# Performance work log

Measured on AMD Instinct MI355X. Metric: run time of the kernel, lower is better.

The kernel has to match this reference:

```python
import jax, jax.numpy as jnp
import numpy as np

N_NODES = 100000
N_EDGES = 800000
N_LABEL = 262144
IN, H, OUT = 16, 256, 128
BN_EPS = 1e-5


def setup_inputs() -> dict:
    key = jax.random.key(0)
    ks = jax.random.split(key, 32)
    def lin(k, fi, fo):
        return jax.random.normal(k, (fi, fo), jnp.float32) / np.sqrt(fi)
    inp = {
        "x": jax.random.normal(ks[0], (N_NODES, IN), jnp.float32),
        "edge_index": jax.random.randint(ks[1], (2, N_EDGES), 0, N_NODES, jnp.int32),
        "edge_weight": jax.random.uniform(ks[2], (N_EDGES,), jnp.float32),
        "edge_label_index": jax.random.randint(ks[3], (2, N_LABEL), 0, N_NODES, jnp.int32),
        # encoder GCN layers: 4 convs, BN on first 3
        "W1": lin(ks[4], IN, H),  "b1": jnp.zeros((H,), jnp.float32),
        "g1": jnp.ones((H,), jnp.float32), "be1": jnp.zeros((H,), jnp.float32),
        "W2": lin(ks[5], H, H),   "b2": jnp.zeros((H,), jnp.float32),
        "g2": jnp.ones((H,), jnp.float32), "be2": jnp.zeros((H,), jnp.float32),
        "W3": lin(ks[6], H, H),   "b3": jnp.zeros((H,), jnp.float32),
        "g3": jnp.ones((H,), jnp.float32), "be3": jnp.zeros((H,), jnp.float32),
        "W4": lin(ks[7], H, OUT), "b4": jnp.zeros((OUT,), jnp.float32),
        # decoder MLP on concatenated pair embeddings
        "D1W": lin(ks[8], 2 * OUT, OUT), "D1b": jnp.zeros((OUT,), jnp.float32),
        "D2W": lin(ks[9], OUT, OUT),     "D2b": jnp.zeros((OUT,), jnp.float32),
        "D3W": lin(ks[10], OUT, 1),      "D3b": jnp.zeros((1,), jnp.float32),
    }
    return inp


def _forward(x, edge_index, edge_weight, edge_label_index,
             W1, b1, g1, be1, W2, b2, g2, be2, W3, b3, g3, be3, W4, b4,
             D1W, D1b, D2W, D2b, D3W, D3b):
    n = x.shape[0]
    src, dst = edge_index[0], edge_index[1]
    # GCN symmetric normalization with self-loops (weight 1)
    deg = jax.ops.segment_sum(edge_weight, dst, num_segments=n) + 1.0
    dinv = jax.lax.rsqrt(deg)
    edge_norm = dinv[src] * edge_weight * dinv[dst]   # [E]
    self_norm = dinv * dinv                            # [N]

    def gcn(h, W, b):
        h = h @ W                                      # [N, F]
        agg = jax.ops.segment_sum(h[src] * edge_norm[:, None], dst, num_segments=n)
        return agg + h * self_norm[:, None] + b

    def bn(h, g, be):  # training-mode BatchNorm1d over node dim
        m = h.mean(axis=0)
        v = h.var(axis=0)
        return (h - m) * jax.lax.rsqrt(v + BN_EPS) * g + be

    h = jax.nn.relu(bn(gcn(x, W1, b1), g1, be1))
    h = jax.nn.relu(bn(gcn(h, W2, b2), g2, be2))
    h = jax.nn.relu(bn(gcn(h, W3, b3), g3, be3))
    z = gcn(h, W4, b4)                                 # [N, OUT] encoded

    # decode: gather both endpoints, concat, MLP + sigmoid
    e0, e1 = edge_label_index[0], edge_label_index[1]
    q = jnp.concatenate([z[e0], z[e1]], axis=1)        # [EL, 2*OUT]
    q = jax.nn.relu(q @ D1W + D1b)
    q = jax.nn.relu(q @ D2W + D2b)
    p = jax.nn.sigmoid(q @ D3W + D3b)
    return p.squeeze(-1)                               # [EL]


def reference(x, edge_index, edge_weight, edge_label_index,
              W1, b1, g1, be1, W2, b2, g2, be2, W3, b3, g3, be3, W4, b4,
              D1W, D1b, D2W, D2b, D3W, D3b):
    return _forward(x, edge_index, edge_weight, edge_label_index,
                    W1, b1, g1, be1, W2, b2, g2, be2, W3, b3, g3, be3, W4, b4,
                    D1W, D1b, D2W, D2b, D3W, D3b)
```

## Files before the change

### kernel.cpp

```cpp
#include <hip/hip_runtime.h>
#include <cmath>

#define NN 100000
#define NE 800000
#define NL 262144
#define GB 782

typedef __attribute__((ext_vector_type(8))) short bf16x8;
typedef __attribute__((ext_vector_type(4))) float f32x4;

__device__ __forceinline__ unsigned short f2bf(float f) {
  unsigned int u = __builtin_bit_cast(unsigned int, f);
  u = (u + 0x7FFF + ((u >> 16) & 1)) >> 16;
  return (unsigned short)u;
}
__device__ __forceinline__ float bf2f(unsigned short u) {
  return __builtin_bit_cast(float, (unsigned int)u << 16);
}

__global__ void k_degcnt(const int* __restrict__ dst, const float* __restrict__ w,
                         unsigned long long* __restrict__ dc) {
  int e = blockIdx.x * 256 + threadIdx.x;
  if (e < NE) {
    unsigned long long pk = (1ULL << 32) | (unsigned long long)(unsigned int)(w[e] * 8388608.0f);
    atomicAdd(&dc[dst[e]], pk);
  }
}
__global__ void k_dinv2(const unsigned long long* __restrict__ dc,
                        float* __restrict__ dinv, int* __restrict__ cnt) {
  int n = blockIdx.x * 256 + threadIdx.x;
  if (n < NN) {
    unsigned long long v = dc[n];
    cnt[n] = (int)(v >> 32);
    dinv[n] = rsqrtf((float)(unsigned int)v * (1.0f / 8388608.0f) + 1.0f);
  }
}
__global__ void k_scan1(const int* __restrict__ cnt, int* __restrict__ tsum) {
  __shared__ int s[256];
  int t = threadIdx.x;
  int base = blockIdx.x * 1024;
  int acc = 0;
  for (int i = 0; i < 4; i++) { int idx = base + t * 4 + i; if (idx < NN) acc += cnt[idx]; }
  s[t] = acc; __syncthreads();
  for (int o = 128; o > 0; o >>= 1) { if (t < o) s[t] += s[t + o]; __syncthreads(); }
  if (t == 0) tsum[blockIdx.x] = s[0];
}
__global__ void k_scan2(const int* __restrict__ tsum, int* __restrict__ toff, int nt, int* __restrict__ rowptr_end) {
  __shared__ int s[256];
  int t = threadIdx.x;
  int v = (t < nt) ? tsum[t] : 0;
  s[t] = v; __syncthreads();
  for (int o = 1; o < 256; o <<= 1) { int xv = (t >= o) ? s[t - o] : 0; __syncthreads(); s[t] += xv; __syncthreads(); }
  if (t < nt) toff[t] = s[t] - v;
  if (t == 255) *rowptr_end = s[255];
}
__global__ void k_scan3(const int* __restrict__ cnt, const int* __restrict__ toff,
                        int* __restrict__ rowptr, int* __restrict__ nxt) {
  __shared__ int s[256];
  int t = threadIdx.x;
  int base = blockIdx.x * 1024 + t * 4;
  int v[4]; int tot = 0;
  for (int i = 0; i < 4; i++) { int idx = base + i; v[i] = (idx < NN) ? cnt[idx] : 0; tot += v[i]; }
  s[t] = tot; __syncthreads();
  for (int o = 1; o < 256; o <<= 1) { int xv = (t >= o) ? s[t - o] : 0; __syncthreads(); s[t] += xv; __syncthreads(); }
  int excl = s[t] - tot + toff[blockIdx.x];
  for (int i = 0; i < 4; i++) {
    int idx = base + i;
    if (idx < NN) { rowptr[idx] = excl; nxt[idx] = excl; }
    excl += v[i];
  }
}
__global__ void k_scatter2(const int* __restrict__ src, const int* __restrict__ dst, const float* __restrict__ w,
                           const float* __restrict__ dinv, int* __restrict__ nxt,
                           int* __restrict__ esp, float* __restrict__ enp) {
  int e = blockIdx.x * 256 + threadIdx.x;
  if (e < NE) {
    int d = dst[e], s = src[e];
    int p = atomicAdd(&nxt[d], 1);
    esp[p] = s; enp[p] = dinv[s] * w[e] * dinv[d];
  }
}

__global__ void k_cvt_wT(const float* __restrict__ W, unsigned short* __restrict__ Wt, int K, int N) {
  int id = blockIdx.x * 256 + threadIdx.x;
  if (id >= K * N) return;
  int n = id / K, k = id - n * K;
  Wt[id] = f2bf(W[k * N + n]);
}

__global__ void k_pack(const unsigned short* __restrict__ Wt, unsigned short* __restrict__ P, int K, int NJ) {
  int id = blockIdx.x * 256 + threadIdx.x;
  int total = (K / 32) * NJ * 64;
  if (id >= total) return;
  int lane = id & 63, g = id >> 6;
  int j = g % NJ, s = g / NJ;
  int fr = lane & 15, fq = lane >> 4;
  uint4 v = *(const uint4*)(Wt + (size_t)(j * 16 + fr) * K + s * 32 + fq * 8);
  *(uint4*)(P + (size_t)id * 8) = v;
}

__global__ __launch_bounds__(256) void k_wuv(const float* __restrict__ W4, const float* __restrict__ D1W,
                                             const float* __restrict__ b4, const float* __restrict__ D1b,
                                             unsigned short* __restrict__ wtUV, float* __restrict__ buv) {
  __shared__ float dc[256];
  int j = blockIdx.x;
  int k = threadIdx.x;
  dc[k] = D1W[k * 128 + j];
  __syncthreads();
  float su = 0.f, sv = 0.f;
  const float* w4r = W4 + k * 128;
  for (int p = 0; p < 128; p++) { float w = w4r[p]; su += w * dc[p]; sv += w * dc[128 + p]; }
  wtUV[(size_t)j * 256 + k] = f2bf(su);
  wtUV[(size_t)(128 + j) * 256 + k] = f2bf(sv);
  if (k == 0) {
    float bu = D1b[j], bv = 0.f;
    for (int p = 0; p < 128; p++) { bu += b4[p] * dc[p]; bv += b4[p] * dc[128 + p]; }
    buv[j] = bu; buv[128 + j] = bv;
  }
}

__global__ __launch_bounds__(256) void k_gemm16(const float* __restrict__ x, const float* __restrict__ W,
                                                unsigned short* __restrict__ out) {
  __shared__ float xs[32][16];
  int t = threadIdx.x; int row0 = blockIdx.x * 32;
  for (int i = t; i < 512; i += 256) {
    int r = i >> 4, c = i & 15; int row = row0 + r;
    xs[r][c] = (row < NN) ? x[(size_t)row * 16 + c] : 0.f;
  }
  float w[16];
  #pragma unroll
  for (int k = 0; k < 16; k++) w[k] = W[k * 256 + t];
  __syncthreads();
  for (int r = 0; r < 32; r++) {
    int row = row0 + r; if (row >= NN) break;
    float acc = 0.f;
    #pragma unroll
    for (int k = 0; k < 16; k++) acc += xs[r][k] * w[k];
    out[(size_t)row * 256 + t] = f2bf(acc);
  }
}

template <bool STATS>
__global__ __launch_bounds__(512) void k_gemm_v8(
    const unsigned short* __restrict__ A, const unsigned short* __restrict__ Wp,
    const float* __restrict__ bias, unsigned short* __restrict__ C,
    float* __restrict__ Ps, float* __restrict__ Pq) {
  __shared__ unsigned short S[128 * 136];
  __shared__ float Ls[256], Lq[256];
  const int t = threadIdx.x;
  const int row0 = blockIdx.x * 128;
  if (STATS && t < 256) { Ls[t] = 0.f; Lq[t] = 0.f; }
  const int lane = t & 63, w = t >> 6, fr = lane & 15, fq = lane >> 4;
  f32x4 acc[16] = {};
  #pragma unroll
  for (int ck = 0; ck < 2; ck++) {
    {
      int r = t >> 2, q = t & 3;
      int row = row0 + r;
      uint4* dst = (uint4*)(S + r * 136 + q * 32);
      if (row < NN) {
        const uint4* src = (const uint4*)(A + (size_t)row * 256 + ck * 128 + q * 32);
        #pragma unroll
        for (int i = 0; i < 4; i++) dst[i] = src[i];
      } else {
        #pragma unroll
        for (int i = 0; i < 4; i++) dst[i] = make_uint4(0, 0, 0, 0);
      }
    }
    __syncthreads();
    #pragma unroll
    for (int s = 0; s < 4; s++) {
      bf16x8 a = *(const bf16x8*)(S + (w * 16 + fr) * 136 + s * 32 + fq * 8);
      const int sg = ck * 4 + s;
      #pragma unroll
      for (int j = 0; j < 16; j++) {
        bf16x8 bw = *(const bf16x8*)(Wp + ((size_t)(sg * 16 + j) * 64 + lane) * 8);
        acc[j] = __builtin_amdgcn_mfma_f32_16x16x32_bf16(a, bw, acc[j], 0, 0, 0);
      }
    }
    __syncthreads();
  }
  #pragma unroll
  for (int j = 0; j < 16; j++) {
    float bj = bias[j * 16 + fr];
    float s_ = 0.f, q_ = 0.f;
    #pragma unroll
    for (int rr = 0; rr < 4; rr++) {
      int row = row0 + w * 16 + fq * 4 + rr;
      if (row < NN) {
        float c = acc[j][rr] + bj;
        C[(size_t)row * 256 + j * 16 + fr] = f2bf(c);
        if (STATS) { s_ += c; q_ += c * c; }
      }
    }
    if (STATS) {
      s_ += __shfl_xor(s_, 16); q_ += __shfl_xor(q_, 16);
      s_ += __shfl_xor(s_, 32); q_ += __shfl_xor(q_, 32);
      if (fq == 0) { atomicAdd(&Ls[j * 16 + fr], s_); atomicAdd(&Lq[j * 16 + fr], q_); }
    }
  }
  if (STATS) {
    __syncthreads();
    if (t < 256) Ps[(size_t)blockIdx.x * 256 + t] = Ls[t];
    else Pq[(size_t)blockIdx.x * 256 + (t - 256)] = Lq[t - 256];
  }
}

__global__ __launch_bounds__(256) void k_bnred(const float* __restrict__ Ps, const float* __restrict__ Pq,
                                               const float* __restrict__ g, const float* __restrict__ be,
                                               float* __restrict__ scale, float* __restrict__ shift) {
  __shared__ float Ss[256], Sq[256];
  const int f = blockIdx.x;
  const int t = threadIdx.x;
  float s = 0.f, q = 0.f;
  for (int p = t; p < GB; p += 256) { s += Ps[(size_t)p * 256 + f]; q += Pq[(size_t)p * 256 + f]; }
  Ss[t] = s; Sq[t] = q;
  __syncthreads();
  for (int o = 128; o > 0; o >>= 1) { if (t < o) { Ss[t] += Ss[t + o]; Sq[t] += Sq[t + o]; } __syncthreads(); }
  if (t == 0) {
    float m = Ss[0] * (1.f / NN);
    float v = Sq[0] * (1.f / NN) - m * m;
    float sc = g[f] * rsqrtf(v + 1e-5f);
    scale[f] = sc; shift[f] = be[f] - m * sc;
  }
}

__device__ __forceinline__ void ld8(const unsigned short* p, float* f) {
  uint4 v = *(const uint4*)p;
  unsigned int u[4] = {v.x, v.y, v.z, v.w};
  #pragma unroll
  for (int i = 0; i < 4; i++) {
    f[2 * i] = bf2f((unsigned short)(u[i] & 0xFFFF));
    f[2 * i + 1] = bf2f((unsigned short)(u[i] >> 16));
  }
}
template <bool BN>
__global__ __launch_bounds__(256) void k_agg5(const unsigned short* __restrict__ hb,
    const int* __restrict__ esp, const float* __restrict__ enp,
    const int* __restrict__ rowptr, const float* __restrict__ dinv,
    const float* __restrict__ scale, const float* __restrict__ shift,
    const float* __restrict__ bias, unsigned short* __restrict__ outb) {
  const int lane = threadIdx.x & 63;
  const int lg = lane & 31;
  const int srcbase = lane & 32;
  const int n = blockIdx.x * 8 + (threadIdx.x >> 5);
  const int f0 = lg * 8;
  float sc8[8] = {}, sh8[8] = {};
  if constexpr (BN) {
    #pragma unroll
    for (int j = 0; j < 8; j++) { sc8[j] = scale[f0 + j]; sh8[j] = shift[f0 + j]; }
  }
  auto xf = [&](float v, int j) -> float {
    if constexpr (BN) return fmaxf(v * sc8[j] + sh8[j], 0.f);
    else return v;
  };
  float d = dinv[n]; float dd = d * d;
  float acc[8];
  {
    float sv[8];
    ld8(hb + (size_t)n * 256 + f0, sv);
    #pragma unroll
    for (int j = 0; j < 8; j++) acc[j] = xf(sv[j], j) * dd + (BN ? 0.f : bias[f0 + j]);
  }
  const int i0 = rowptr[n];
  const int dg = rowptr[n + 1] - i0;
  int sreg = 0; float wreg = 0.f;
  if (lg < dg) { sreg = esp[i0 + lg]; wreg = enp[i0 + lg]; }
  const int m = (dg < 32) ? dg : 32;
  int e = 0;
  for (; e + 4 <= m; e += 4) {
    int s0 = __shfl(sreg, srcbase | e), s1 = __shfl(sreg, srcbase | (e + 1));
    int s2 = __shfl(sreg, srcbase | (e + 2)), s3 = __shfl(sreg, srcbase | (e + 3));
    float w0 = __shfl(wreg, srcbase | e), w1 = __shfl(wreg, srcbase | (e + 1));
    float w2 = __shfl(wreg, srcbase | (e + 2)), w3 = __shfl(wreg, srcbase | (e + 3));
    float r0[8], r1[8], r2[8], r3[8];
    ld8(hb + (size_t)s0 * 256 + f0, r0);
    ld8(hb + (size_t)s1 * 256 + f0, r1);
    ld8(hb + (size_t)s2 * 256 + f0, r2);
    ld8(hb + (size_t)s3 * 256 + f0, r3);
    #pragma unroll
    for (int j = 0; j < 8; j++)
      acc[j] += w0 * xf(r0[j], j) + w1 * xf(r1[j], j) + w2 * xf(r2[j], j) + w3 * xf(r3[j], j);
  }
  for (; e < m; e++) {
    int s0 = __shfl(sreg, srcbase | e); float w0 = __shfl(wreg, srcbase | e);
    float r0[8];
    ld8(hb + (size_t)s0 * 256 + f0, r0);
    #pragma unroll
    for (int j = 0; j < 8; j++) acc[j] += w0 * xf(r0[j], j);
  }
  for (int i = i0 + 32; i < i0 + dg; i++) {
    int s0 = esp[i]; float w0 = enp[i];
    float r0[8];
    ld8(hb + (size_t)s0 * 256 + f0, r0);
    #pragma unroll
    for (int j = 0; j < 8; j++) acc[j] += w0 * xf(r0[j], j);
  }
  unsigned int o[4];
  #pragma unroll
  for (int i = 0; i < 4; i++)
    o[i] = (unsigned int)f2bf(acc[2 * i]) | ((unsigned int)f2bf(acc[2 * i + 1]) << 16);
  *(uint4*)(outb + (size_t)n * 256 + f0) = make_uint4(o[0], o[1], o[2], o[3]);
}

__global__ __launch_bounds__(256) void k_bnstats2(const unsigned short* __restrict__ h,
                                                  float* __restrict__ sums, float* __restrict__ sqs) {
  __shared__ float L[4][256];
  int t = threadIdx.x;
  int fp = t & 127;
  size_t rbase = (size_t)blockIdx.x * 256 + (t >> 7);
  float s0 = 0, q0 = 0, s1 = 0, q1 = 0;
  for (int i = 0; i < 128; i++) {
    size_t r = rbase + 2 * (size_t)i;
    if (r >= NN) break;
    unsigned int v = *(const unsigned int*)&h[r * 256 + fp * 2];
    float a = bf2f((unsigned short)(v & 0xFFFF));
    float b = bf2f((unsigned short)(v >> 16));
    s0 += a; q0 += a * a; s1 += b; q1 += b * b;
  }
  L[0][t] = s0; L[1][t] = q0; L[2][t] = s1; L[3][t] = q1;
  __syncthreads();
  if (t < 128) {
    s0 = L[0][t] + L[0][t + 128]; q0 = L[1][t] + L[1][t + 128];
    s1 = L[2][t] + L[2][t + 128]; q1 = L[3][t] + L[3][t + 128];
    atomicAdd(&sums[2 * t], s0); atomicAdd(&sqs[2 * t], q0);
    atomicAdd(&sums[2 * t + 1], s1); atomicAdd(&sqs[2 * t + 1], q1);
  }
}
__global__ void k_bnfinal(const float* __restrict__ sums, const float* __restrict__ sqs,
                          const float* __restrict__ g, const float* __restrict__ be,
                          float* __restrict__ scale, float* __restrict__ shift) {
  int f = threadIdx.x;
  float m = sums[f] * (1.f / NN);
  float v = sqs[f] * (1.f / NN) - m * m;
  float sc = g[f] * rsqrtf(v + 1e-5f);
  scale[f] = sc; shift[f] = be[f] - m * sc;
}

__global__ __launch_bounds__(256) void k_decoder3(
    const unsigned short* __restrict__ uv,
    const int* __restrict__ l0, const int* __restrict__ l1,
    const unsigned short* __restrict__ W2p, const float* __restrict__ D2b,
    const float* __restrict__ D3W, const float* __restrict__ D3b,
    float* __restrict__ out) {
  __shared__ unsigned short S[128 * 136];
  __shared__ int ei0[128], ei1[128];
  const int t = threadIdx.x;
  const int base = blockIdx.x * 128;
  if (t < 128) ei0[t] = l0[base + t];
  else ei1[t - 128] = l1[base + t - 128];
  __syncthreads();
  {
    int e = t >> 1, h = t & 1;
    const uint4* pu = (const uint4*)(uv + (size_t)ei0[e] * 256 + h * 64);
    const uint4* pv = (const uint4*)(uv + (size_t)ei1[e] * 256 + 128 + h * 64);
    uint4* dst = (uint4*)(S + e * 136 + h * 64);
    #pragma unroll
    for (int i = 0; i < 8; i++) {
      uint4 a = pu[i], b = pv[i];
      unsigned int ia[4] = {a.x, a.y, a.z, a.w};
      unsigned int ib[4] = {b.x, b.y, b.z, b.w};
      unsigned int o[4];
      #pragma unroll
      for (int p = 0; p < 4; p++) {
        float lo = fmaxf(bf2f((unsigned short)(ia[p] & 0xFFFF)) + bf2f((unsigned short)(ib[p] & 0xFFFF)), 0.f);
        float hi = fmaxf(bf2f((unsigned short)(ia[p] >> 16)) + bf2f((unsigned short)(ib[p] >> 16)), 0.f);
        o[p] = (unsigned int)f2bf(lo) | ((unsigned int)f2bf(hi) << 16);
      }
      dst[i] = make_uint4(o[0], o[1], o[2], o[3]);
    }
  }
  __syncthreads();
  const int lane = t & 63, w = t >> 6, fr = lane & 15, fq = lane >> 4;
  f32x4 acc2[2][8] = {};
  #pragma unroll
  for (int s = 0; s < 4; s++) {
    bf16x8 a0 = *(const bf16x8*)(S + (w * 32 + fr) * 136 + s * 32 + fq * 8);
    bf16x8 a1 = *(const bf16x8*)(S + (w * 32 + 16 + fr) * 136 + s * 32 + fq * 8);
    #pragma unroll
    for (int j = 0; j < 8; j++) {
      bf16x8 bw = *(const bf16x8*)(W2p + ((size_t)(s * 8 + j) * 64 + lane) * 8);
      acc2[0][j] = __builtin_amdgcn_mfma_f32_16x16x32_bf16(a0, bw, acc2[0][j], 0, 0, 0);
      acc2[1][j] = __builtin_amdgcn_mfma_f32_16x16x32_bf16(a1, bw, acc2[1][j], 0, 0, 0);
    }
  }
  float b2v[8], w3v[8];
  #pragma unroll
  for (int j = 0; j < 8; j++) { b2v[j] = D2b[j * 16 + fr]; w3v[j] = D3W[j * 16 + fr]; }
  float d3b = D3b[0];
  #pragma unroll
  for (int f = 0; f < 2; f++) {
    float p[4] = {0.f, 0.f, 0.f, 0.f};
    #pragma unroll
    for (int j = 0; j < 8; j++)
      #pragma unroll
      for (int r = 0; r < 4; r++)
        p[r] += fmaxf(acc2[f][j][r] + b2v[j], 0.f) * w3v[j];
    #pragma unroll
    for (int r = 0; r < 4; r++) {
      p[r] += __shfl_xor(p[r], 1);
      p[r] += __shfl_xor(p[r], 2);
      p[r] += __shfl_xor(p[r], 4);
      p[r] += __shfl_xor(p[r], 8);
      if (fr == 0) out[base + w * 32 + f * 16 + fq * 4 + r] = 1.f / (1.f + expf(-(p[r] + d3b)));
    }
  }
}

extern "C" void kernel_launch(void* const* d_in, const int* in_sizes, int n_in,
                              void* d_out, int out_size, void* d_ws, size_t ws_size,
                              hipStream_t stream) {
  const float* x = (const float*)d_in[0];
  const int* ei = (const int*)d_in[1];
  const int* esrc = ei; const int* edst = ei + NE;
  const float* ew = (const float*)d_in[2];
  const int* eli = (const int*)d_in[3];
  const int* l0 = eli; const int* l1 = eli + NL;
  const float* W1 = (const float*)d_in[4],  *b1 = (const float*)d_in[5];
  const float* g1 = (const float*)d_in[6],  *be1 = (const float*)d_in[7];
  const float* W2 = (const float*)d_in[8],  *b2 = (const float*)d_in[9];
  const float* g2 = (const float*)d_in[10], *be2 = (const float*)d_in[11];
  const float* W3 = (const float*)d_in[12], *b3 = (const float*)d_in[13];
  const float* g3 = (const float*)d_in[14], *be3 = (const float*)d_in[15];
  const float* W4 = (const float*)d_in[16], *b4 = (const float*)d_in[17];
  const float* D1W = (const float*)d_in[18], *D1b = (const float*)d_in[19];
  const float* D2W = (const float*)d_in[20], *D2b = (const float*)d_in[21];
  const float* D3W = (const float*)d_in[22], *D3b = (const float*)d_in[23];
  float* out = (float*)d_out;

  float* wf = (float*)d_ws;
  size_t off = 0;
  auto A = [&](size_t n) { float* p = wf + off; off += (n + 63) & ~(size_t)63; return p; };
  float* dinv = A(NN);
  float* enp = A(NE);
  float* sums = A(256);
  float* sqs = A(256);
  float* scale = A(256);
  float* shift = A(256);
  float* buv = A(256);
  float* Ps = A((size_t)GB * 256);
  float* Pq = A((size_t)GB * 256);
  unsigned long long* dc = (unsigned long long*)A(2 * (size_t)NN);
  int* cnt = (int*)A(NN);
  int* rowptr = (int*)A(NN + 1);
  int* nxt = (int*)A(NN);
  int* esp = (int*)A(NE);
  int* tsum = (int*)A(256);
  int* toff = (int*)A(256);
  unsigned short* hbA = (unsigned short*)A((size_t)NN * 128);
  unsigned short* hbB = (unsigned short*)A((size_t)NN * 128);
  unsigned short* uv  = (unsigned short*)A((size_t)NN * 128);
  unsigned short* wt2 = (unsigned short*)A(256 * 128);
  unsigned short* wt3 = (unsigned short*)A(256 * 128);
  unsigned short* wtUV = (unsigned short*)A(256 * 128);
  unsigned short* w2t = (unsigned short*)A(64 * 128);
  unsigned short* wp2 = (unsigned short*)A(256 * 128);
  unsigned short* wp3 = (unsigned short*)A(256 * 128);
  unsigned short* wpUV = (unsigned short*)A(256 * 128);
  unsigned short* w2p = (unsigned short*)A(64 * 128);

  const int EB = (NE + 255) / 256;
  const int NB = (NN + 255) / 256;
  const int ST = (NN + 1023) / 1024;
  const int AB = NN / 8;

  hipMemsetAsync(dc, 0, (size_t)NN * 8, stream);
  k_degcnt<<<EB, 256, 0, stream>>>(edst, ew, dc);
  k_dinv2<<<NB, 256, 0, stream>>>(dc, dinv, cnt);
  k_scan1<<<ST, 256, 0, stream>>>(cnt, tsum);
  k_scan2<<<1, 256, 0, stream>>>(tsum, toff, ST, rowptr + NN);
  k_scan3<<<ST, 256, 0, stream>>>(cnt, toff, rowptr, nxt);
  k_scatter2<<<EB, 256, 0, stream>>>(esrc, edst, ew, dinv, nxt, esp, enp);

  k_cvt_wT<<<(256 * 256 + 255) / 256, 256, 0, stream>>>(W2, wt2, 256, 256);
  k_cvt_wT<<<(256 * 256 + 255) / 256, 256, 0, stream>>>(W3, wt3, 256, 256);
  k_cvt_wT<<<(128 * 128 + 255) / 256, 256, 0, stream>>>(D2W, w2t, 128, 128);
  k_wuv<<<128, 256, 0, stream>>>(W4, D1W, b4, D1b, wtUV, buv);
  k_pack<<<32, 256, 0, stream>>>(wt2, wp2, 256, 16);
  k_pack<<<32, 256, 0, stream>>>(wt3, wp3, 256, 16);
  k_pack<<<32, 256, 0, stream>>>(wtUV, wpUV, 256, 16);
  k_pack<<<8, 256, 0, stream>>>(w2t, w2p, 128, 8);

  k_gemm16<<<(NN + 31) / 32, 256, 0, stream>>>(x, W1, hbA);
  k_agg5<false><<<AB, 256, 0, stream>>>(hbA, esp, enp, rowptr, dinv, nullptr, nullptr, b1, hbB);
  hipMemsetAsync(sums, 0, 512 * sizeof(float), stream);
  k_bnstats2<<<NB, 256, 0, stream>>>(hbB, sums, sqs);
  k_bnfinal<<<1, 256, 0, stream>>>(sums, sqs, g1, be1, scale, shift);

  k_agg5<true><<<AB, 256, 0, stream>>>(hbB, esp, enp, rowptr, dinv, scale, shift, nullptr, hbA);
  k_gemm_v8<true><<<GB, 512, 0, stream>>>(hbA, wp2, b2, hbB, Ps, Pq);
  k_bnred<<<256, 256, 0, stream>>>(Ps, Pq, g2, be2, scale, shift);

  k_agg5<true><<<AB, 256, 0, stream>>>(hbB, esp, enp, rowptr, dinv, scale, shift, nullptr, hbA);
  k_gemm_v8<true><<<GB, 512, 0, stream>>>(hbA, wp3, b3, hbB, Ps, Pq);
  k_bnred<<<256, 256, 0, stream>>>(Ps, Pq, g3, be3, scale, shift);

  k_agg5<true><<<AB, 256, 0, stream>>>(hbB, esp, enp, rowptr, dinv, scale, shift, nullptr, hbA);
  k_gemm_v8<false><<<GB, 512, 0, stream>>>(hbA, wpUV, buv, uv, nullptr, nullptr);

  k_decoder3<<<NL / 128, 256, 0, stream>>>(uv, l0, l1, w2p, D2b, D3W, D3b, out);
}
```

Before: 730.4 us.

## Restructure GEMM so each wave owns column slice with register-resident weights

The GEMM kernel now loads the full 128x256 A tile into LDS at once, and each wave keeps its 32-column slice of the packed weights in registers. Previously each wave owned 16 rows and reloaded all 256 columns of weights from global memory on every k-step. The per-block BN partial sums are now written directly from the owning wave, which removes the LDS atomics and an extra barrier. The tradeoffs are higher register pressure (16 B fragments plus 16 accumulators) and more LDS per block, which may reduce occupancy.

Result: faster. 708.5 us (-3.0%).

```diff
diff --git a/kernel.cpp b/kernel.cpp
--- a/kernel.cpp
+++ b/kernel.cpp
@@ -141,68 +141,69 @@
 }
 
 template <bool STATS>
-__global__ __launch_bounds__(512) void k_gemm_v8(
+__global__ __launch_bounds__(512) void k_gemm_v12(
     const unsigned short* __restrict__ A, const unsigned short* __restrict__ Wp,
     const float* __restrict__ bias, unsigned short* __restrict__ C,
     float* __restrict__ Ps, float* __restrict__ Pq) {
-  __shared__ unsigned short S[128 * 136];
-  __shared__ float Ls[256], Lq[256];
+  __shared__ unsigned short S[128 * 264];
   const int t = threadIdx.x;
+  const int lane = t & 63, w = t >> 6, fr = lane & 15, fq = lane >> 4;
   const int row0 = blockIdx.x * 128;
-  if (STATS && t < 256) { Ls[t] = 0.f; Lq[t] = 0.f; }
-  const int lane = t & 63, w = t >> 6, fr = lane & 15, fq = lane >> 4;
-  f32x4 acc[16] = {};
-  #pragma unroll
-  for (int ck = 0; ck < 2; ck++) {
-    {
-      int r = t >> 2, q = t & 3;
-      int row = row0 + r;
-      uint4* dst = (uint4*)(S + r * 136 + q * 32);
-      if (row < NN) {
-        const uint4* src = (const uint4*)(A + (size_t)row * 256 + ck * 128 + q * 32);
-        #pragma unroll
-        for (int i = 0; i < 4; i++) dst[i] = src[i];
-      } else {
-        #pragma unroll
-        for (int i = 0; i < 4; i++) dst[i] = make_uint4(0, 0, 0, 0);
-      }
-    }
-    __syncthreads();
-    #pragma unroll
-    for (int s = 0; s < 4; s++) {
-      bf16x8 a = *(const bf16x8*)(S + (w * 16 + fr) * 136 + s * 32 + fq * 8);
-      const int sg = ck * 4 + s;
+  bf16x8 B0[8], B1[8];
+  #pragma unroll
+  for (int s = 0; s < 8; s++) {
+    B0[s] = *(const bf16x8*)(Wp + ((size_t)(s * 16 + 2 * w) * 64 + lane) * 8);
+    B1[s] = *(const bf16x8*)(Wp + ((size_t)(s * 16 + 2 * w + 1) * 64 + lane) * 8);
+  }
+  {
+    int r = t >> 2, q = t & 3;
+    int row = row0 + r;
+    uint4* dst = (uint4*)(S + r * 264 + q * 64);
+    if (row < NN) {
+      const uint4* src = (const uint4*)(A + (size_t)row * 256 + q * 64);
       #pragma unroll
-      for (int j = 0; j < 16; j++) {
-        bf16x8 bw = *(const bf16x8*)(Wp + ((size_t)(sg * 16 + j) * 64 + lane) * 8);
-        acc[j] = __builtin_amdgcn_mfma_f32_16x16x32_bf16(a, bw, acc[j], 0, 0, 0);
-      }
-    }
-    __syncthreads();
-  }
-  #pragma unroll
-  for (int j = 0; j < 16; j++) {
-    float bj = bias[j * 16 + fr];
+      for (int i = 0; i < 8; i++) dst[i] = src[i];
+    } else {
+      #pragma unroll
+      for (int i = 0; i < 8; i++) dst[i] = make_uint4(0, 0, 0, 0);
+    }
+  }
+  __syncthreads();
+  f32x4 acc[8][2] = {};
+  #pragma unroll
+  for (int r = 0; r < 8; r++) {
+    #pragma unroll
+    for (int s = 0; s < 8; s++) {
+      bf16x8 a = *(const bf16x8*)(S + (r * 16 + fr) * 264 + s * 32 + fq * 8);
+      acc[r][0] = __builtin_amdgcn_mfma_f32_16x16x32_bf16(a, B0[s], acc[r][0], 0, 0, 0);
+      acc[r][1] = __builtin_amdgcn_mfma_f32_16x16x32_bf16(a, B1[s], acc[r][1], 0, 0, 0);
+    }
+  }
+  #pragma unroll
+  for (int jl = 0; jl < 2; jl++) {
+    const int col = w * 32 + jl * 16 + fr;
+    float bj = bias[col];
     float s_ = 0.f, q_ = 0.f;
     #pragma unroll
-    for (int rr = 0; rr < 4; rr++) {
-      int row = row0 + w * 16 + fq * 4 + rr;
-      if (row < NN) {
-        float c = acc[j][rr] + bj;
-        C[(size_t)row * 256 + j * 16 + fr] = f2bf(c);
-        if (STATS) { s_ += c; q_ += c * c; }
+    for (int r = 0; r < 8; r++) {
+      #pragma unroll
+      for (int rr = 0; rr < 4; rr++) {
+        int row = row0 + r * 16 + fq * 4 + rr;
+        if (row < NN) {
+          float c = acc[r][jl][rr] + bj;
+          C[(size_t)row * 256 + col] = f2bf(c);
+          if (STATS) { s_ += c; q_ += c * c; }
+        }
       }
     }
     if (STATS) {
       s_ += __shfl_xor(s_, 16); q_ += __shfl_xor(q_, 16);
       s_ += __shfl_xor(s_, 32); q_ += __shfl_xor(q_, 32);
-      if (fq == 0) { atomicAdd(&Ls[j * 16 + fr], s_); atomicAdd(&Lq[j * 16 + fr], q_); }
-    }
-  }
-  if (STATS) {
-    __syncthreads();
-    if (t < 256) Ps[(size_t)blockIdx.x * 256 + t] = Ls[t];
-    else Pq[(size_t)blockIdx.x * 256 + (t - 256)] = Lq[t - 256];
+      if (fq == 0) {
+        Ps[(size_t)blockIdx.x * 256 + col] = s_;
+        Pq[(size_t)blockIdx.x * 256 + col] = q_;
+      }
+    }
   }
 }
 
@@ -488,15 +489,15 @@
   k_bnfinal<<<1, 256, 0, stream>>>(sums, sqs, g1, be1, scale, shift);
 
   k_agg5<true><<<AB, 256, 0, stream>>>(hbB, esp, enp, rowptr, dinv, scale, shift, nullptr, hbA);
-  k_gemm_v8<true><<<GB, 512, 0, stream>>>(hbA, wp2, b2, hbB, Ps, Pq);
+  k_gemm_v12<true><<<GB, 512, 0, stream>>>(hbA, wp2, b2, hbB, Ps, Pq);
   k_bnred<<<256, 256, 0, stream>>>(Ps, Pq, g2, be2, scale, shift);
 
   k_agg5<true><<<AB, 256, 0, stream>>>(hbB, esp, enp, rowptr, dinv, scale, shift, nullptr, hbA);
-  k_gemm_v8<true><<<GB, 512, 0, stream>>>(hbA, wp3, b3, hbB, Ps, Pq);
+  k_gemm_v12<true><<<GB, 512, 0, stream>>>(hbA, wp3, b3, hbB, Ps, Pq);
   k_bnred<<<256, 256, 0, stream>>>(Ps, Pq, g3, be3, scale, shift);
 
   k_agg5<true><<<AB, 256, 0, stream>>>(hbB, esp, enp, rowptr, dinv, scale, shift, nullptr, hbA);
-  k_gemm_v8<false><<<GB, 512, 0, stream>>>(hbA, wpUV, buv, uv, nullptr, nullptr);
+  k_gemm_v12<false><<<GB, 512, 0, stream>>>(hbA, wpUV, buv, uv, nullptr, nullptr);
 
   k_decoder3<<<NL / 128, 256, 0, stream>>>(uv, l0, l1, w2p, D2b, D3W, D3b, out);
 }
```
